# Kernel tuning notes

Measured on AMD Instinct MI355X. Metric: run time of the kernel, lower is better.

The kernel has to match this reference:

```python
import jax, jax.numpy as jnp
import numpy as np

MARGIN = 0.3
EPS = 1e-12


def setup_inputs() -> dict:
    key = jax.random.key(0)
    k1, k2, k3 = jax.random.split(key, 3)
    B, D = 8192, 1024
    features = jax.random.normal(k1, (B, D), dtype=jnp.float32)
    labels = jax.random.randint(k2, (B,), 0, 100, dtype=jnp.int64)
    domain_labels = jax.random.randint(k3, (B,), 0, 2, dtype=jnp.int64)
    return {"features": features, "labels": labels, "domain_labels": domain_labels}


def reference(features, labels, domain_labels):
    # L2-normalize rows (F.normalize: x / max(||x||, eps))
    norm = jnp.maximum(jnp.linalg.norm(features, axis=1, keepdims=True), EPS)
    f = features / norm

    herb = domain_labels == 0   # [B] anchors
    field = domain_labels == 1  # [B] candidates

    sq = jnp.sum(f * f, axis=1)                                   # [B]
    d2 = sq[:, None] + sq[None, :] - 2.0 * jnp.einsum('id,jd->ij', f, f)
    d = jnp.sqrt(jnp.maximum(d2, 0.0))                            # [B, B]

    same = labels[:, None] == labels[None, :]                     # [B, B]
    pair = herb[:, None] & field[None, :]
    pos_mask = pair & same
    neg_mask = pair & ~same

    INF = jnp.float32(jnp.inf)
    pos_min = jnp.min(jnp.where(pos_mask, d, INF), axis=1)        # [B]
    neg_min = jnp.min(jnp.where(neg_mask, d, INF), axis=1)        # [B]

    valid = herb & jnp.any(pos_mask, axis=1) & jnp.any(neg_mask, axis=1)
    # Substitute 0 for invalid rows BEFORE subtracting to avoid inf - inf.
    pos_s = jnp.where(valid, pos_min, 0.0)
    neg_s = jnp.where(valid, neg_min, 0.0)
    tl = jnp.maximum(pos_s - neg_s + MARGIN, 0.0)                 # [B]

    loss_sum = jnp.sum(jnp.where(valid, tl, 0.0))
    count = jnp.sum(valid.astype(jnp.float32))
    return jnp.where(count > 0, loss_sum / jnp.maximum(count, 1.0), 0.0)
```

## Files before the change

kernel.cpp:

```cpp
#include <hip/hip_runtime.h>


#define B_ROWS 8192
#define DIM    1024

typedef __bf16 bf16x8 __attribute__((ext_vector_type(8)));
typedef float  f32x4  __attribute__((ext_vector_type(4)));

__device__ __forceinline__ unsigned short f2bf_rne(float x) {
    unsigned u = __float_as_uint(x);
    unsigned r = (u + 0x7FFFu + ((u >> 16) & 1u)) >> 16;
    return (unsigned short)r;
}
__device__ __forceinline__ float bf2f(unsigned short h) {
    return __uint_as_float(((unsigned)h) << 16);
}

__global__ __launch_bounds__(256) void compute_slots(
    const int* __restrict__ dom, int* __restrict__ slotOf,
    unsigned* __restrict__ cnt)
{
    __shared__ int cnts[256];
    __shared__ int base[257];
    const int t = threadIdx.x;
    const int p0 = t * 32;

    unsigned mask = 0u; int c = 0;
    #pragma unroll
    for (int i = 0; i < 32; ++i) {
        const int isA = (dom[p0 + i] == 0) ? 1 : 0;
        mask |= ((unsigned)isA) << i;
        c += isA;
    }
    cnts[t] = c;
    __syncthreads();
    if (t == 0) {
        int acc = 0;
        for (int i = 0; i < 256; ++i) { base[i] = acc; acc += cnts[i]; }
        base[256] = acc;
        cnt[0] = (unsigned)acc;
    }
    __syncthreads();
    const int nA = base[256];
    int aB = base[t];
    #pragma unroll
    for (int i = 0; i < 32; ++i) {
        const int isA = (mask >> i) & 1;
        slotOf[p0 + i] = isA ? aB : nA + (p0 + i - aB);
        aB += isA;
    }
}

__global__ __launch_bounds__(256) void normalize_rows(
    const float* __restrict__ feat, const int* __restrict__ labels,
    const int* __restrict__ slotOf, unsigned short* __restrict__ G,
    int* __restrict__ labG, float* __restrict__ sqG)
{
    const int wv = threadIdx.x >> 6, lane = threadIdx.x & 63;
    const int row = blockIdx.x * 4 + wv;

    const float4* src = (const float4*)(feat + (size_t)row * DIM);
    float4 v[4];
    float ss = 0.0f;
    #pragma unroll
    for (int j = 0; j < 4; ++j) {
        v[j] = src[j * 64 + lane];
        ss += v[j].x * v[j].x + v[j].y * v[j].y + v[j].z * v[j].z + v[j].w * v[j].w;
    }
    #pragma unroll
    for (int s = 32; s > 0; s >>= 1) ss += __shfl_xor(ss, s);
    const float inv = 1.0f / fmaxf(sqrtf(ss), 1e-12f);

    const int slot = slotOf[row];
    unsigned short ub[16];
    float ss2 = 0.0f;
    #pragma unroll
    for (int j = 0; j < 4; ++j) {
        const float f0 = v[j].x * inv, f1 = v[j].y * inv,
                    f2 = v[j].z * inv, f3 = v[j].w * inv;
        ub[j * 4 + 0] = f2bf_rne(f0); ub[j * 4 + 1] = f2bf_rne(f1);
        ub[j * 4 + 2] = f2bf_rne(f2); ub[j * 4 + 3] = f2bf_rne(f3);
        #pragma unroll
        for (int q = 0; q < 4; ++q) {
            const float fr = bf2f(ub[j * 4 + q]);
            ss2 += fr * fr;
        }
    }
    #pragma unroll
    for (int s = 32; s > 0; s >>= 1) ss2 += __shfl_xor(ss2, s);
    if (lane == 0) {
        sqG[slot]  = ss2;
        labG[slot] = labels[row];
    }
    ushort4* dst = (ushort4*)(G + (size_t)slot * DIM);
    #pragma unroll
    for (int j = 0; j < 4; ++j) {
        ushort4 pk;
        pk.x = ub[j * 4 + 0]; pk.y = ub[j * 4 + 1];
        pk.z = ub[j * 4 + 2]; pk.w = ub[j * 4 + 3];
        dst[j * 64 + lane] = pk;
    }
}

__global__ __launch_bounds__(256) void tile_mindist(
    const unsigned short* __restrict__ G, const int* __restrict__ labG,
    const float* __restrict__ sqG, const unsigned* __restrict__ cnt,
    unsigned* __restrict__ posmin, unsigned* __restrict__ negmin)
{
    const int nA = (int)cnt[0];
    const int nF = B_ROWS - nA;
    const int nTA = (nA + 127) >> 7;
    const int nTF = (nF + 127) >> 7;
    const int total = nTA * nTF;

    __shared__ __align__(16) unsigned short S[2][2][128 * 40];

    const int t = threadIdx.x;
    const int lane = t & 63, w = t >> 6;
    const int wm = w >> 1, wn = w & 1;
    const int l15 = lane & 15, quad = lane >> 4;

    const int r0 = t >> 2;
    const int cByte = (t & 3) * 16;
    const int wOff0 = r0 * 40 + (cByte >> 1);
    const int wOff1 = (r0 + 64) * 40 + (cByte >> 1);
    const int rdA = (wm * 64 + l15) * 40 + quad * 8;
    const int rdF = (wn * 64 + l15) * 40 + quad * 8;

    const char* Gb = (const char*)G;

    for (int tile = blockIdx.x; tile < total; tile += gridDim.x) {
        const int tx = tile % nTA;
        const int ty = tile / nTA;
        const int rowA0 = tx * 128;
        const int rowF0 = nA + ty * 128;

        int rF0c = rowF0 + r0;       if (rF0c > B_ROWS - 1) rF0c = B_ROWS - 1;
        int rF1c = rowF0 + r0 + 64;  if (rF1c > B_ROWS - 1) rF1c = B_ROWS - 1;
        const char* gA0 = Gb + (size_t)(rowA0 + r0) * (DIM * 2) + cByte;
        const char* gA1 = gA0 + (size_t)64 * (DIM * 2);
        const char* gF0 = Gb + (size_t)rF0c * (DIM * 2) + cByte;
        const char* gF1 = Gb + (size_t)rF1c * (DIM * 2) + cByte;

        f32x4 acc[4][4] = {};

        {
            const uint4 a0 = *(const uint4*)(gA0);
            const uint4 a1 = *(const uint4*)(gA1);
            const uint4 f0 = *(const uint4*)(gF0);
            const uint4 f1 = *(const uint4*)(gF1);
            *(uint4*)&S[0][0][wOff0] = a0;
            *(uint4*)&S[0][0][wOff1] = a1;
            *(uint4*)&S[0][1][wOff0] = f0;
            *(uint4*)&S[0][1][wOff1] = f1;
        }
        __syncthreads();

        #pragma unroll 4
        for (int step = 0; step < 32; ++step) {
            const int cur = step & 1;
            const bool has_next = step < 31;
            uint4 na0, na1, nf0, nf1;
            if (has_next) {
                const int off = (step + 1) * 64;
                na0 = *(const uint4*)(gA0 + off);
                na1 = *(const uint4*)(gA1 + off);
                nf0 = *(const uint4*)(gF0 + off);
                nf1 = *(const uint4*)(gF1 + off);
            }

            const unsigned short* pa = &S[cur][0][rdA];
            const unsigned short* pf = &S[cur][1][rdF];
            bf16x8 a[4], b[4];
            #pragma unroll
            for (int fm = 0; fm < 4; ++fm) a[fm] = *(const bf16x8*)(pa + fm * 640);
            #pragma unroll
            for (int fn = 0; fn < 4; ++fn) b[fn] = *(const bf16x8*)(pf + fn * 640);
            #pragma unroll
            for (int fm = 0; fm < 4; ++fm)
                #pragma unroll
                for (int fn = 0; fn < 4; ++fn)
                    acc[fm][fn] = __builtin_amdgcn_mfma_f32_16x16x32_bf16(
                        a[fm], b[fn], acc[fm][fn], 0, 0, 0);

            if (has_next) {
                const int nb = cur ^ 1;
                *(uint4*)&S[nb][0][wOff0] = na0;
                *(uint4*)&S[nb][0][wOff1] = na1;
                *(uint4*)&S[nb][1][wOff0] = nf0;
                *(uint4*)&S[nb][1][wOff1] = nf1;
            }
            __syncthreads();
        }

        const float INFV = __uint_as_float(0x7f800000u);
        float sqf[4]; int lf_[4]; bool vf[4];
        #pragma unroll
        for (int fn = 0; fn < 4; ++fn) {
            const int rf = rowF0 + wn * 64 + fn * 16 + l15;
            vf[fn] = rf < B_ROWS;
            const int rc = vf[fn] ? rf : (B_ROWS - 1);
            sqf[fn] = sqG[rc];
            lf_[fn] = labG[rc];
        }
        #pragma unroll
        for (int fm = 0; fm < 4; ++fm) {
            #pragma unroll
            for (int r = 0; r < 4; ++r) {
                const int ra = rowA0 + wm * 64 + fm * 16 + quad * 4 + r;
                const bool va = ra < nA;
                const int rac = va ? ra : 0;
                const float sqa = sqG[rac];
                const int la_ = labG[rac];
                float pmin = INFV, nmin = INFV;
                #pragma unroll
                for (int fn = 0; fn < 4; ++fn) {
                    const float dd = fmaxf(sqa + sqf[fn] - 2.0f * acc[fm][fn][r], 0.0f);
                    if (vf[fn]) {
                        if (la_ == lf_[fn]) pmin = fminf(pmin, dd);
                        else                nmin = fminf(nmin, dd);
                    }
                }
                #pragma unroll
                for (int s = 1; s < 16; s <<= 1) {
                    pmin = fminf(pmin, __shfl_xor(pmin, s));
                    nmin = fminf(nmin, __shfl_xor(nmin, s));
                }
                if (l15 == 0 && va) {
                    if (pmin < INFV) atomicMin(&posmin[ra], __float_as_uint(pmin));
                    if (nmin < INFV) atomicMin(&negmin[ra], __float_as_uint(nmin));
                }
            }
        }
    }
}

__global__ __launch_bounds__(256) void reduce_loss(
    const unsigned* __restrict__ posmin, const unsigned* __restrict__ negmin,
    float* __restrict__ accum)
{
    const int i = blockIdx.x * 256 + threadIdx.x;
    const unsigned up = posmin[i], un = negmin[i];
    float tl = 0.0f, c = 0.0f;
    if (up != 0xFFFFFFFFu && un != 0xFFFFFFFFu) {
        const float pd = sqrtf(__uint_as_float(up));
        const float nd = sqrtf(__uint_as_float(un));
        tl = fmaxf(pd - nd + 0.3f, 0.0f);
        c = 1.0f;
    }
    #pragma unroll
    for (int s = 32; s > 0; s >>= 1) {
        tl += __shfl_down(tl, s);
        c  += __shfl_down(c, s);
    }
    __shared__ float sb[8];
    const int lane = threadIdx.x & 63, w = threadIdx.x >> 6;
    if (lane == 0) { sb[w] = tl; sb[4 + w] = c; }
    __syncthreads();
    if (threadIdx.x == 0) {
        atomicAdd(&accum[0], sb[0] + sb[1] + sb[2] + sb[3]);
        atomicAdd(&accum[1], sb[4] + sb[5] + sb[6] + sb[7]);
    }
}

__global__ void finalize(const float* __restrict__ accum, float* __restrict__ out) {
    const float s = accum[0], c = accum[1];
    out[0] = (c > 0.0f) ? s / fmaxf(c, 1.0f) : 0.0f;
}

extern "C" void kernel_launch(void* const* d_in, const int* in_sizes, int n_in,
                              void* d_out, int out_size, void* d_ws, size_t ws_size,
                              hipStream_t stream) {
    const float* feat  = (const float*)d_in[0];
    const int* labels  = (const int*)d_in[1];
    const int* dom     = (const int*)d_in[2];
    float* out = (float*)d_out;

    char* ws = (char*)d_ws;
    unsigned short* G   = (unsigned short*)(ws);
    int*      labG      = (int*)(ws + 16777216);
    float*    sqG       = (float*)(ws + 16809984);
    unsigned* posmin    = (unsigned*)(ws + 16842752);
    unsigned* negmin    = (unsigned*)(ws + 16875520);
    unsigned* cnt       = (unsigned*)(ws + 16908288);
    float*    accum     = (float*)(ws + 16908296);
    int*      slotOf    = (int*)(ws + 16842752);

    hipMemsetAsync(cnt, 0, 16, stream);

    compute_slots<<<1, 256, 0, stream>>>(dom, slotOf, cnt);
    normalize_rows<<<B_ROWS / 4, 256, 0, stream>>>(feat, labels, slotOf,
                                                   G, labG, sqG);

    hipMemsetAsync(posmin, 0xFF, 65536, stream);

    tile_mindist<<<1056, 256, 0, stream>>>(G, labG, sqG, cnt, posmin, negmin);

    reduce_loss<<<B_ROWS / 256, 256, 0, stream>>>(posmin, negmin, accum);
    finalize<<<1, 1, 0, stream>>>(accum, out);
}
```

Baseline: 188.2 us.

## Stage GEMM tiles into LDS with direct global_load_lds async copies

Replaces the register-staged global-to-LDS prefetch in the distance GEMM with `__builtin_amdgcn_global_load_lds` 16-byte copies. These write straight into the next double-buffer slot while MFMAs run on the current slot. The LDS tile drops its padding (row stride 40 to 32 halfwords) so each wave's contiguous DMA chunk maps to 16 rows, and a barrier is added at the end of each tile. This is meant to save VGPRs and the store instructions in the main loop. The risk is more LDS bank conflicts on the unpadded `bf16x8` reads and correct wait ordering for the async loads.

```diff
diff --git a/kernel.cpp b/kernel.cpp
--- a/kernel.cpp
+++ b/kernel.cpp
@@ -14,6 +14,13 @@
 }
 __device__ __forceinline__ float bf2f(unsigned short h) {
     return __uint_as_float(((unsigned)h) << 16);
+}
+
+__device__ __forceinline__ void async_copy16(const void* g, void* l) {
+    __builtin_amdgcn_global_load_lds(
+        (const __attribute__((address_space(1))) unsigned int*)g,
+        (__attribute__((address_space(3))) unsigned int*)l,
+        16, 0, 0);
 }
 
 __global__ __launch_bounds__(256) void compute_slots(
@@ -113,19 +120,19 @@
     const int nTF = (nF + 127) >> 7;
     const int total = nTA * nTF;
 
-    __shared__ __align__(16) unsigned short S[2][2][128 * 40];
+    __shared__ __align__(16) unsigned short S[2][2][128 * 32];
 
     const int t = threadIdx.x;
     const int lane = t & 63, w = t >> 6;
     const int wm = w >> 1, wn = w & 1;
     const int l15 = lane & 15, quad = lane >> 4;
 
-    const int r0 = t >> 2;
-    const int cByte = (t & 3) * 16;
-    const int wOff0 = r0 * 40 + (cByte >> 1);
-    const int wOff1 = (r0 + 64) * 40 + (cByte >> 1);
-    const int rdA = (wm * 64 + l15) * 40 + quad * 8;
-    const int rdF = (wn * 64 + l15) * 40 + quad * 8;
+    const int ch0 = 2 * w;
+    const int crow = lane >> 2;
+    const int cbyte = (lane & 3) * 16;
+
+    const int rdA = (wm * 64 + l15) * 32 + quad * 8;
+    const int rdF = (wn * 64 + l15) * 32 + quad * 8;
 
     const char* Gb = (const char*)G;
 
@@ -135,47 +142,46 @@
         const int rowA0 = tx * 128;
         const int rowF0 = nA + ty * 128;
 
-        int rF0c = rowF0 + r0;       if (rF0c > B_ROWS - 1) rF0c = B_ROWS - 1;
-        int rF1c = rowF0 + r0 + 64;  if (rF1c > B_ROWS - 1) rF1c = B_ROWS - 1;
-        const char* gA0 = Gb + (size_t)(rowA0 + r0) * (DIM * 2) + cByte;
-        const char* gA1 = gA0 + (size_t)64 * (DIM * 2);
-        const char* gF0 = Gb + (size_t)rF0c * (DIM * 2) + cByte;
-        const char* gF1 = Gb + (size_t)rF1c * (DIM * 2) + cByte;
+        const char* ga[2]; const char* gf[2];
+        #pragma unroll
+        for (int h = 0; h < 2; ++h) {
+            const int ch = ch0 + h;
+            const int rA = rowA0 + 16 * ch + crow;
+            int rF = rowF0 + 16 * ch + crow;
+            if (rF > B_ROWS - 1) rF = B_ROWS - 1;
+            ga[h] = Gb + (size_t)rA * (DIM * 2) + cbyte;
+            gf[h] = Gb + (size_t)rF * (DIM * 2) + cbyte;
+        }
 
         f32x4 acc[4][4] = {};
 
-        {
-            const uint4 a0 = *(const uint4*)(gA0);
-            const uint4 a1 = *(const uint4*)(gA1);
-            const uint4 f0 = *(const uint4*)(gF0);
-            const uint4 f1 = *(const uint4*)(gF1);
-            *(uint4*)&S[0][0][wOff0] = a0;
-            *(uint4*)&S[0][0][wOff1] = a1;
-            *(uint4*)&S[0][1][wOff0] = f0;
-            *(uint4*)&S[0][1][wOff1] = f1;
+        #pragma unroll
+        for (int h = 0; h < 2; ++h) {
+            async_copy16(ga[h], &S[0][0][(ch0 + h) * 512]);
+            async_copy16(gf[h], &S[0][1][(ch0 + h) * 512]);
         }
         __syncthreads();
 
         #pragma unroll 4
         for (int step = 0; step < 32; ++step) {
             const int cur = step & 1;
-            const bool has_next = step < 31;
-            uint4 na0, na1, nf0, nf1;
-            if (has_next) {
+            const int nb = cur ^ 1;
+            if (step < 31) {
                 const int off = (step + 1) * 64;
-                na0 = *(const uint4*)(gA0 + off);
-                na1 = *(const uint4*)(gA1 + off);
-                nf0 = *(const uint4*)(gF0 + off);
-                nf1 = *(const uint4*)(gF1 + off);
+                #pragma unroll
+                for (int h = 0; h < 2; ++h) {
+                    async_copy16(ga[h] + off, &S[nb][0][(ch0 + h) * 512]);
+                    async_copy16(gf[h] + off, &S[nb][1][(ch0 + h) * 512]);
+                }
             }
 
             const unsigned short* pa = &S[cur][0][rdA];
             const unsigned short* pf = &S[cur][1][rdF];
             bf16x8 a[4], b[4];
             #pragma unroll
-            for (int fm = 0; fm < 4; ++fm) a[fm] = *(const bf16x8*)(pa + fm * 640);
+            for (int fm = 0; fm < 4; ++fm) a[fm] = *(const bf16x8*)(pa + fm * 512);
             #pragma unroll
-            for (int fn = 0; fn < 4; ++fn) b[fn] = *(const bf16x8*)(pf + fn * 640);
+            for (int fn = 0; fn < 4; ++fn) b[fn] = *(const bf16x8*)(pf + fn * 512);
             #pragma unroll
             for (int fm = 0; fm < 4; ++fm)
                 #pragma unroll
@@ -183,13 +189,6 @@
                     acc[fm][fn] = __builtin_amdgcn_mfma_f32_16x16x32_bf16(
                         a[fm], b[fn], acc[fm][fn], 0, 0, 0);
 
-            if (has_next) {
-                const int nb = cur ^ 1;
-                *(uint4*)&S[nb][0][wOff0] = na0;
-                *(uint4*)&S[nb][0][wOff1] = na1;
-                *(uint4*)&S[nb][1][wOff0] = nf0;
-                *(uint4*)&S[nb][1][wOff1] = nf1;
-            }
             __syncthreads();
         }
 
@@ -232,6 +231,7 @@
                 }
             }
         }
+        __syncthreads();
     }
 }
 
```

Result: faster. 180.5 us (-4.1%).
